# Performance work log

Measured on AMD Instinct MI355X. Metric: run time of the kernel, lower is better.

Reference implementation:

```python
import jax, jax.numpy as jnp
import numpy as np

N = 4096        # num_nodes == num_messages (required by the einsum contraction)
HID = 256       # hidden_dim
MD = 32         # message_dim (per-head dim)
H = 8           # num_heads


def setup_inputs() -> dict:
    key = jax.random.key(0)
    ks = jax.random.split(key, 12)
    s = 0.02
    return {
        "node_features": jax.random.normal(ks[0], (N, HID), dtype=jnp.float32),
        "messages": jax.random.normal(ks[1], (N, MD), dtype=jnp.float32),
        "adjacency": jax.random.randint(ks[2], (N, N), 0, 2, dtype=jnp.int32),
        "Wq": jax.random.normal(ks[3], (HID, H * MD), dtype=jnp.float32) * s,
        "bq": jnp.zeros((H * MD,), dtype=jnp.float32),
        "Wk": jax.random.normal(ks[4], (HID, H * MD), dtype=jnp.float32) * s,
        "bk": jnp.zeros((H * MD,), dtype=jnp.float32),
        "Wv": jax.random.normal(ks[5], (MD, H * MD), dtype=jnp.float32) * s,
        "bv": jnp.zeros((H * MD,), dtype=jnp.float32),
        "Wo": jax.random.normal(ks[6], (H * MD, MD), dtype=jnp.float32) * s,
        "bo": jnp.zeros((MD,), dtype=jnp.float32),
    }


def reference(node_features, messages, adjacency, Wq, bq, Wk, bk, Wv, bv, Wo, bo):
    n = node_features.shape[0]
    m = messages.shape[0]
    # projections; view(num, H, -1) splits the H*MD output as [H, MD]
    Q = (node_features @ Wq + bq).reshape(n, H, MD)   # [n, h, d]
    K = (node_features @ Wk + bk).reshape(n, H, MD)   # [m, h, d] (m == n)
    V = (messages @ Wv + bv).reshape(m, H, MD)        # [m, h, d]
    scale = 1.0 / np.sqrt(MD).astype(np.float32)
    scores = jnp.einsum('nhd,mhd->nmh', Q, K) * scale  # [n, m, h]
    # adjacency mask: masked_fill(mask == 0, -1e9)
    scores = jnp.where((adjacency == 0)[:, :, None], jnp.float32(-1e9), scores)
    attn = jax.nn.softmax(scores, axis=1)              # softmax over m
    routed = jnp.einsum('nmh,mhd->nhd', attn, V).reshape(n, H * MD)
    routed = routed @ Wo + bo                          # [n, MD]
    return routed, attn.mean(axis=-1)                  # ([n, MD], [n, m])
```

## Files before the change

### kernel.cpp

```cpp
#include <hip/hip_runtime.h>
#include <math.h>

#define NN 4096
#define HID 256
#define MD 32
#define NH 8
#define SCALE 0.17677669529663687f

typedef float f32x4 __attribute__((ext_vector_type(4)));
typedef short bf16x8 __attribute__((ext_vector_type(8)));
typedef _Float16 f16x4 __attribute__((ext_vector_type(4)));
typedef _Float16 f16x2 __attribute__((ext_vector_type(2)));

__device__ inline unsigned int bfr(float x) {
    unsigned int u = __float_as_uint(x);
    return (u + 0x7fffu + ((u >> 16) & 1u)) >> 16;
}
__device__ inline unsigned int pkbf(float a, float b) {
    return bfr(a) | (bfr(b) << 16);
}
__device__ inline unsigned int pkhf(float a, float b) {
    union { f16x2 h; unsigned int u; } z;
    z.h = (f16x2){(_Float16)a, (_Float16)b};
    return z.u;
}
__device__ inline unsigned int spread4(unsigned int x) {
    x = (x | (x << 12)) & 0x000F000Fu;
    x = (x | (x << 6))  & 0x03030303u;
    x = (x | (x << 3))  & 0x11111111u;
    return x;
}

__global__ __launch_bounds__(256) void prep_kernel(
    const float* __restrict__ nf, const float* __restrict__ Wq,
    const float* __restrict__ Wk, unsigned short* __restrict__ NFb,
    unsigned short* __restrict__ Wt)
{
    __shared__ __align__(16) float lds[64 * 65];
    const int b = blockIdx.x, t = threadIdx.x;
    if (b < 512) {
        const float* src = nf + (size_t)b * 2048 + t * 8;
        float4 a = ((const float4*)src)[0];
        float4 c = ((const float4*)src)[1];
        uint4 o;
        o.x = pkbf(a.x, a.y); o.y = pkbf(a.z, a.w);
        o.z = pkbf(c.x, c.y); o.w = pkbf(c.z, c.w);
        *(uint4*)(NFb + (size_t)b * 2048 + t * 8) = o;
        return;
    }
    const int b2 = b - 512;
    const int mat = b2 >> 4, tile = b2 & 15;
    const int k0 = (tile >> 2) * 64, c0 = (tile & 3) * 64;
    const float* W = mat ? Wk : Wq;
    #pragma unroll
    for (int i = 0; i < 16; ++i) {
        int idx = i * 256 + t;
        int row = idx >> 4, c4 = idx & 15;
        float4 v = *(const float4*)(W + (size_t)(k0 + row) * 256 + c0 + c4 * 4);
        lds[row * 65 + c4 * 4 + 0] = v.x;
        lds[row * 65 + c4 * 4 + 1] = v.y;
        lds[row * 65 + c4 * 4 + 2] = v.z;
        lds[row * 65 + c4 * 4 + 3] = v.w;
    }
    __syncthreads();
    #pragma unroll
    for (int i = 0; i < 2; ++i) {
        int j = i * 256 + t;
        int c_loc = j >> 3, kq = j & 7;
        uint4 o;
        o.x = pkbf(lds[(kq * 8 + 0) * 65 + c_loc], lds[(kq * 8 + 1) * 65 + c_loc]);
        o.y = pkbf(lds[(kq * 8 + 2) * 65 + c_loc], lds[(kq * 8 + 3) * 65 + c_loc]);
        o.z = pkbf(lds[(kq * 8 + 4) * 65 + c_loc], lds[(kq * 8 + 5) * 65 + c_loc]);
        o.w = pkbf(lds[(kq * 8 + 6) * 65 + c_loc], lds[(kq * 8 + 7) * 65 + c_loc]);
        *(uint4*)(Wt + (size_t)mat * 65536 + (size_t)(c0 + c_loc) * 256 + k0 + kq * 8) = o;
    }
}

__global__ __launch_bounds__(256, 4) void proj_mfma(
    const unsigned short* __restrict__ NFb, const unsigned short* __restrict__ Wt,
    const float* __restrict__ bq, const float* __restrict__ bk,
    unsigned short* __restrict__ Qb, unsigned short* __restrict__ Kb)
{
    const int b = blockIdx.x;
    const int isK = b >> 7, nb = b & 127;
    const unsigned short* Wm = Wt + (size_t)isK * 65536;
    const float* bias = isK ? bk : bq;
    unsigned short* outp = isK ? Kb : Qb;
    const int t = threadIdx.x, w = t >> 6, l = t & 63;
    const int g = l >> 4, q = l & 15;
    const int n0 = nb * 32 + (w & 1) * 16;
    const int chalf = w >> 1;

    f32x4 acc[8];
    #pragma unroll
    for (int ct = 0; ct < 8; ++ct) acc[ct] = (f32x4){0.f, 0.f, 0.f, 0.f};

    #pragma unroll
    for (int kc = 0; kc < 8; ++kc) {
        bf16x8 bfrag = *(const bf16x8*)(NFb + (size_t)(n0 + q) * 256 + kc * 32 + g * 8);
        #pragma unroll
        for (int ct = 0; ct < 8; ++ct) {
            int c = (chalf * 8 + ct) * 16 + q;
            bf16x8 afrag = *(const bf16x8*)(Wm + (size_t)c * 256 + kc * 32 + g * 8);
            acc[ct] = __builtin_amdgcn_mfma_f32_16x16x32_bf16(afrag, bfrag, acc[ct], 0, 0, 0);
        }
    }
    const float sc = isK ? 1.0f : SCALE;
    const int n = n0 + q;
    #pragma unroll
    for (int ct = 0; ct < 8; ++ct) {
        int c0 = (chalf * 8 + ct) * 16 + 4 * g;
        float4 bv = *(const float4*)(bias + c0);
        float v0 = (acc[ct][0] + bv.x) * sc;
        float v1 = (acc[ct][1] + bv.y) * sc;
        float v2 = (acc[ct][2] + bv.z) * sc;
        float v3 = (acc[ct][3] + bv.w) * sc;
        uint2 o;
        o.x = pkbf(v0, v1); o.y = pkbf(v2, v3);
        int h = c0 >> 5, d = c0 & 31;
        *(uint2*)(outp + ((size_t)h * NN + n) * 32 + d) = o;
    }
}

__global__ __launch_bounds__(256) void proj_v(
    const float* __restrict__ msg, const float* __restrict__ Wv,
    const float* __restrict__ bv, float* __restrict__ Vo)
{
    __shared__ __align__(16) float in_lds[32 * 32];
    const int nb = blockIdx.x;
    const int t = threadIdx.x;
    ((float4*)in_lds)[t] = ((const float4*)(msg + (size_t)nb * 1024))[t];
    __syncthreads();
    float acc[32];
    #pragma unroll
    for (int r = 0; r < 32; ++r) acc[r] = 0.f;
    #pragma unroll 8
    for (int k = 0; k < 32; ++k) {
        float w = Wv[k * 256 + t];
        #pragma unroll
        for (int r = 0; r < 32; ++r) acc[r] += in_lds[r * 32 + k] * w;
    }
    const float bb = bv[t];
    #pragma unroll
    for (int r = 0; r < 32; ++r)
        Vo[(size_t)(nb * 32 + r) * 256 + t] = acc[r] + bb;
}

__global__ __launch_bounds__(256) void abit_kernel(
    const int* __restrict__ adj, unsigned int* __restrict__ ab32)
{
    const int w = threadIdx.x >> 6, lane = threadIdx.x & 63;
    const int n = blockIdx.x * 4 + w;
    const int* base = adj + (size_t)n * NN;
    for (int it = 0; it < 16; ++it) {
        int4 v = *(const int4*)(base + it * 256 + lane * 4);
        unsigned long long b0 = __ballot(v.x != 0);
        unsigned long long b1 = __ballot(v.y != 0);
        unsigned long long b2 = __ballot(v.z != 0);
        unsigned long long b3 = __ballot(v.w != 0);
        if (lane < 8) {
            unsigned int sh = lane * 8;
            unsigned int B0 = (unsigned int)((b0 >> sh) & 0xffULL);
            unsigned int B1 = (unsigned int)((b1 >> sh) & 0xffULL);
            unsigned int B2 = (unsigned int)((b2 >> sh) & 0xffULL);
            unsigned int B3 = (unsigned int)((b3 >> sh) & 0xffULL);
            unsigned int wd = spread4(B0) | (spread4(B1) << 1)
                            | (spread4(B2) << 2) | (spread4(B3) << 3);
            ab32[(size_t)n * 128 + it * 8 + lane] = wd;
        }
    }
}

__global__ __launch_bounds__(256) void pack_vt(
    const float* __restrict__ Vf, unsigned short* __restrict__ Vt, int usef16)
{
    __shared__ __align__(16) float lds[128 * 33];
    const int h = blockIdx.x >> 5, mt = blockIdx.x & 31;
    const int t = threadIdx.x;
    for (int k = 0; k < 4; ++k) {
        int flat = k * 256 + t;
        int row = flat >> 3, c4 = flat & 7;
        float4 v = *(const float4*)(Vf + (size_t)(mt * 128 + row) * 256 + h * 32 + c4 * 4);
        lds[row * 33 + c4 * 4 + 0] = v.x;
        lds[row * 33 + c4 * 4 + 1] = v.y;
        lds[row * 33 + c4 * 4 + 2] = v.z;
        lds[row * 33 + c4 * 4 + 3] = v.w;
    }
    __syncthreads();
    const int d = t >> 3, mq = t & 7;
    #pragma unroll
    for (int k = 0; k < 2; ++k) {
        int m0 = mq * 16 + k * 8;
        uint4 o;
        if (usef16) {
            o.x = pkhf(lds[(m0 + 0) * 33 + d], lds[(m0 + 1) * 33 + d]);
            o.y = pkhf(lds[(m0 + 2) * 33 + d], lds[(m0 + 3) * 33 + d]);
            o.z = pkhf(lds[(m0 + 4) * 33 + d], lds[(m0 + 5) * 33 + d]);
            o.w = pkhf(lds[(m0 + 6) * 33 + d], lds[(m0 + 7) * 33 + d]);
        } else {
            o.x = pkbf(lds[(m0 + 0) * 33 + d], lds[(m0 + 1) * 33 + d]);
            o.y = pkbf(lds[(m0 + 2) * 33 + d], lds[(m0 + 3) * 33 + d]);
            o.z = pkbf(lds[(m0 + 4) * 33 + d], lds[(m0 + 5) * 33 + d]);
            o.w = pkbf(lds[(m0 + 6) * 33 + d], lds[(m0 + 7) * 33 + d]);
        }
        *(uint4*)(Vt + ((size_t)(h * 32 + d)) * NN + mt * 128 + m0) = o;
    }
}

__global__ __launch_bounds__(256, 4) void sweep1s_kernel(
    const unsigned short* __restrict__ Qb, const unsigned short* __restrict__ Kb,
    const unsigned int* __restrict__ abit, float* __restrict__ Lpart)
{
    __shared__ __align__(16) char smem[32768];
    const int nquad = blockIdx.x, msg = blockIdx.y;
    const int t = threadIdx.x;
    const int w = t >> 6, l = t & 63;
    const int g = l >> 4, q = l & 15;
    const int n0 = nquad * 64 + w * 16;
    const int m0 = msg * 512;
    const int fq = (q >> 1) & 3;

    const char* gsrc[4];
    #pragma unroll
    for (int i = 0; i < 4; ++i) {
        int s = i * 256 + t;
        int tile = s >> 7;
        int r = (s >> 2) & 31;
        int gr = (s & 3) ^ ((r >> 1) & 3);
        gsrc[i] = (const char*)Kb + (((size_t)tile * NN + m0 + r) * 64 + gr * 16);
    }
    const unsigned int* abrow = abit + (size_t)(n0 + q) * 128 + msg * 16;

    bf16x8 qf[8];
    #pragma unroll
    for (int h = 0; h < 8; ++h)
        qf[h] = *(const bf16x8*)(Qb + (((size_t)h * NN + n0 + q) << 5) + g * 8);
    float lacc[8];
    #pragma unroll
    for (int h = 0; h < 8; ++h) lacc[h] = 0.f;

    #pragma unroll
    for (int i = 0; i < 4; ++i)
        __builtin_amdgcn_global_load_lds((const unsigned int*)gsrc[i],
            (unsigned int*)(smem + i * 4096 + w * 1024), 16, 0, 0);
    unsigned int wb = abrow[0];
    unsigned int wbn = 0;
    __syncthreads();

    for (int c = 0; c < 16; ++c) {
        const char* cur = smem + (c & 1) * 16384;
        if (c < 15) {
            wbn = abrow[c + 1];
            char* nxt = smem + ((c & 1) ^ 1) * 16384;
            #pragma unroll
            for (int i = 0; i < 4; ++i)
                __builtin_amdgcn_global_load_lds(
                    (const unsigned int*)(gsrc[i] + (size_t)(c + 1) * 2048),
                    (unsigned int*)(nxt + i * 4096 + w * 1024), 16, 0, 0);
        }
        #pragma unroll
        for (int h = 0; h < 8; ++h) {
            const int ko = h * 2048 + q * 64 + ((g ^ fq) << 4);
            bf16x8 ka0 = *(const bf16x8*)(cur + ko);
            bf16x8 ka1 = *(const bf16x8*)(cur + ko + 1024);
            f32x4 z = {0.f, 0.f, 0.f, 0.f};
            f32x4 s0 = __builtin_amdgcn_mfma_f32_16x16x32_bf16(ka0, qf[h], z, 0, 0, 0);
            f32x4 s1 = __builtin_amdgcn_mfma_f32_16x16x32_bf16(ka1, qf[h], z, 0, 0, 0);
            #pragma unroll
            for (int r = 0; r < 4; ++r) {
                float e0 = __expf(s0[r]);
                float e1 = __expf(s1[r]);
                lacc[h] += ((wb >> (4 * g + r)) & 1u) ? e0 : 0.f;
                lacc[h] += ((wb >> (16 + 4 * g + r)) & 1u) ? e1 : 0.f;
            }
        }
        __syncthreads();
        wb = wbn;
    }
    #pragma unroll
    for (int h = 0; h < 8; ++h) {
        float v = lacc[h];
        v += __shfl_xor(v, 16);
        v += __shfl_xor(v, 32);
        if (g == 0) Lpart[(size_t)msg * 32768 + h * NN + n0 + q] = v;
    }
}

__global__ __launch_bounds__(256, 2) void sweep2s_kernel(
    const unsigned short* __restrict__ Qb, const unsigned short* __restrict__ Kb,
    const unsigned short* __restrict__ Vt, const unsigned int* __restrict__ abit,
    const float* __restrict__ Linv, float* __restrict__ Opart,
    float* __restrict__ amean)
{
    __shared__ __align__(16) char smem[65536];
    const int nquad = blockIdx.x, msg = blockIdx.y;
    const int t = threadIdx.x;
    const int w = t >> 6, l = t & 63;
    const int g = l >> 4, q = l & 15;
    const int n0 = nquad * 64 + w * 16;
    const int m0 = msg * 512;
    const int fq = (q >> 1) & 3;

    const char* gsrc[8];
    unsigned int gstep[8];
    #pragma unroll
    for (int i = 0; i < 8; ++i) {
        int s = i * 256 + t;
        int tile = s >> 7;
        int r = (s >> 2) & 31;
        int gr = (s & 3) ^ ((r >> 1) & 3);
        if (tile < 8) {
            gsrc[i] = (const char*)Kb + (((size_t)tile * NN + m0 + r) * 64 + gr * 16);
            gstep[i] = 2048;
        } else {
            gsrc[i] = (const char*)Vt + ((((size_t)(tile - 8) * 32 + r) * NN + m0) * 2 + gr * 16);
            gstep[i] = 64;
        }
    }
    const unsigned int* abrow = abit + (size_t)(n0 + q) * 128 + msg * 16;

    bf16x8 qf[8];
    float rL[8];
    #pragma unroll
    for (int h = 0; h < 8; ++h) {
        qf[h] = *(const bf16x8*)(Qb + (((size_t)h * NN + n0 + q) << 5) + g * 8);
        rL[h] = Linv[h * NN + n0 + q];
    }
    f32x4 o[8][2];
    #pragma unroll
    for (int h = 0; h < 8; ++h) {
        o[h][0] = (f32x4){0.f, 0.f, 0.f, 0.f};
        o[h][1] = (f32x4){0.f, 0.f, 0.f, 0.f};
    }

    #pragma unroll
    for (int i = 0; i < 8; ++i)
        __builtin_amdgcn_global_load_lds((const unsigned int*)gsrc[i],
            (unsigned int*)(smem + i * 4096 + w * 1024), 16, 0, 0);
    unsigned int wb = abrow[0];
    unsigned int wbn = 0;
    __syncthreads();

    for (int c = 0; c < 16; ++c) {
        const char* cur = smem + (c & 1) * 32768;
        if (c < 15) {
            wbn = abrow[c + 1];
            char* nxt = smem + ((c & 1) ^ 1) * 32768;
            #pragma unroll
            for (int i = 0; i < 8; ++i)
                __builtin_amdgcn_global_load_lds(
                    (const unsigned int*)(gsrc[i] + (size_t)(c + 1) * gstep[i]),
                    (unsigned int*)(nxt + i * 4096 + w * 1024), 16, 0, 0);
        }
        const int mb = m0 + c * 32;
        float am[8];
        #pragma unroll
        for (int r = 0; r < 8; ++r) am[r] = 0.f;

        #pragma unroll
        for (int h = 0; h < 8; ++h) {
            const int ko = h * 2048 + q * 64 + ((g ^ fq) << 4);
            bf16x8 ka0 = *(const bf16x8*)(cur + ko);
            bf16x8 ka1 = *(const bf16x8*)(cur + ko + 1024);
            const int vbase = (8 + h) * 2048 + q * 64 + (g & 1) * 8;
            const int vo0 = vbase + (((g >> 1) ^ fq) << 4);
            const int vo1 = vbase + (((2 + (g >> 1)) ^ fq) << 4);
            f16x4 va00 = *(const f16x4*)(cur + vo0);
            f16x4 va01 = *(const f16x4*)(cur + vo0 + 1024);
            f16x4 va10 = *(const f16x4*)(cur + vo1);
            f16x4 va11 = *(const f16x4*)(cur + vo1 + 1024);
            f32x4 z = {0.f, 0.f, 0.f, 0.f};
            f32x4 s0 = __builtin_amdgcn_mfma_f32_16x16x32_bf16(ka0, qf[h], z, 0, 0, 0);
            f32x4 s1 = __builtin_amdgcn_mfma_f32_16x16x32_bf16(ka1, qf[h], z, 0, 0, 0);
            float pn[8];
            #pragma unroll
            for (int r = 0; r < 4; ++r) {
                float e0 = __expf(s0[r]) * rL[h];
                float e1 = __expf(s1[r]) * rL[h];
                pn[r]     = ((wb >> (4 * g + r)) & 1u) ? e0 : 0.f;
                pn[4 + r] = ((wb >> (16 + 4 * g + r)) & 1u) ? e1 : 0.f;
                am[r] += pn[r];
                am[4 + r] += pn[4 + r];
            }
            union { unsigned int u[2]; f16x4 v; } pA, pB;
            pA.u[0] = pkhf(pn[0], pn[1]); pA.u[1] = pkhf(pn[2], pn[3]);
            pB.u[0] = pkhf(pn[4], pn[5]); pB.u[1] = pkhf(pn[6], pn[7]);
            o[h][0] = __builtin_amdgcn_mfma_f32_16x16x16f16(va00, pA.v, o[h][0], 0, 0, 0);
            o[h][1] = __builtin_amdgcn_mfma_f32_16x16x16f16(va01, pA.v, o[h][1], 0, 0, 0);
            o[h][0] = __builtin_amdgcn_mfma_f32_16x16x16f16(va10, pB.v, o[h][0], 0, 0, 0);
            o[h][1] = __builtin_amdgcn_mfma_f32_16x16x16f16(va11, pB.v, o[h][1], 0, 0, 0);
        }
        float4 a0, a1;
        a0.x = am[0] * 0.125f; a0.y = am[1] * 0.125f;
        a0.z = am[2] * 0.125f; a0.w = am[3] * 0.125f;
        a1.x = am[4] * 0.125f; a1.y = am[5] * 0.125f;
        a1.z = am[6] * 0.125f; a1.w = am[7] * 0.125f;
        *(float4*)(amean + (size_t)(n0 + q) * NN + mb + 4 * g) = a0;
        *(float4*)(amean + (size_t)(n0 + q) * NN + mb + 16 + 4 * g) = a1;
        __syncthreads();
        wb = wbn;
    }

    float* op = Opart + ((size_t)msg * NN + n0 + q) * 256;
    #pragma unroll
    for (int h = 0; h < 8; ++h) {
        *(f32x4*)(op + h * 32 + 4 * g) = o[h][0];
        *(f32x4*)(op + h * 32 + 16 + 4 * g) = o[h][1];
    }
}

__global__ __launch_bounds__(256, 4) void sweep1_old(
    const unsigned short* __restrict__ Qb, const unsigned short* __restrict__ Kb,
    const unsigned int* __restrict__ abit, float* __restrict__ Lpart)
{
    const int ntile = blockIdx.x, msg = blockIdx.y;
    const int t = threadIdx.x;
    const int w = t >> 6, l = t & 63;
    const int g = l >> 4, q = l & 15;
    const int ms = msg * 4 + w;
    const int n0 = ntile * 16;
    const int mbase = ms * 256;
    bf16x8 qf[8];
    #pragma unroll
    for (int h = 0; h < 8; ++h)
        qf[h] = *(const bf16x8*)(Qb + (((size_t)h * NN + n0 + q) << 5) + g * 8);
    float lacc[8];
    #pragma unroll
    for (int h = 0; h < 8; ++h) lacc[h] = 0.f;
    for (int ch = 0; ch < 8; ++ch) {
        const int mb = mbase + ch * 32;
        const unsigned int wbits = abit[(size_t)(n0 + q) * 128 + (mb >> 5)];
        #pragma unroll
        for (int h = 0; h < 8; ++h) {
            bf16x8 ka0 = *(const bf16x8*)(Kb + (((size_t)h * NN + mb + q) << 5) + g * 8);
            bf16x8 ka1 = *(const bf16x8*)(Kb + (((size_t)h * NN + mb + 16 + q) << 5) + g * 8);
            f32x4 z = {0.f, 0.f, 0.f, 0.f};
            f32x4 s0 = __builtin_amdgcn_mfma_f32_16x16x32_bf16(ka0, qf[h], z, 0, 0, 0);
            f32x4 s1 = __builtin_amdgcn_mfma_f32_16x16x32_bf16(ka1, qf[h], z, 0, 0, 0);
            #pragma unroll
            for (int r = 0; r < 4; ++r) {
                float e0 = __expf(s0[r]);
                float e1 = __expf(s1[r]);
                lacc[h] += ((wbits >> (4 * g + r)) & 1u) ? e0 : 0.f;
                lacc[h] += ((wbits >> (16 + 4 * g + r)) & 1u) ? e1 : 0.f;
            }
        }
    }
    #pragma unroll
    for (int h = 0; h < 8; ++h) {
        float v = lacc[h];
        v += __shfl_xor(v, 16);
        v += __shfl_xor(v, 32);
        if (g == 0) Lpart[(size_t)ms * 32768 + h * NN + n0 + q] = v;
    }
}

__global__ __launch_bounds__(256, 2) void sweep2_old(
    const unsigned short* __restrict__ Qb, const unsigned short* __restrict__ Kb,
    const unsigned short* __restrict__ Vt, const unsigned int* __restrict__ abit,
    const float* __restrict__ Linv, float* __restrict__ Opart,
    float* __restrict__ amean)
{
    __shared__ __align__(16) float Ow[2 * 16 * 260];
    const int ntile = blockIdx.x, msg = blockIdx.y;
    const int t = threadIdx.x;
    const int w = t >> 6, l = t & 63;
    const int g = l >> 4, q = l & 15;
    const int ms = msg * 4 + w;
    const int n0 = ntile * 16;
    const int mbase = ms * 256;
    const int baddr = (q + (g & 1) * 32) << 2;
    const bool hi = (g >= 2);
    bf16x8 qf[8];
    float rL[8];
    #pragma unroll
    for (int h = 0; h < 8; ++h) {
        qf[h] = *(const bf16x8*)(Qb + (((size_t)h * NN + n0 + q) << 5) + g * 8);
        rL[h] = Linv[h * NN + n0 + q];
    }
    f32x4 o[8][2];
    #pragma unroll
    for (int h = 0; h < 8; ++h) {
        o[h][0] = (f32x4){0.f, 0.f, 0.f, 0.f};
        o[h][1] = (f32x4){0.f, 0.f, 0.f, 0.f};
    }
    for (int ch = 0; ch < 8; ++ch) {
        const int mb = mbase + ch * 32;
        const unsigned int wbits = abit[(size_t)(n0 + q) * 128 + (mb >> 5)];
        float am[8];
        #pragma unroll
        for (int r = 0; r < 8; ++r) am[r] = 0.f;
        #pragma unroll
        for (int h = 0; h < 8; ++h) {
            bf16x8 ka0 = *(const bf16x8*)(Kb + (((size_t)h * NN + mb + q) << 5) + g * 8);
            bf16x8 ka1 = *(const bf16x8*)(Kb + (((size_t)h * NN + mb + 16 + q) << 5) + g * 8);
            f32x4 z = {0.f, 0.f, 0.f, 0.f};
            f32x4 s0 = __builtin_amdgcn_mfma_f32_16x16x32_bf16(ka0, qf[h], z, 0, 0, 0);
            f32x4 s1 = __builtin_amdgcn_mfma_f32_16x16x32_bf16(ka1, qf[h], z, 0, 0, 0);
            float pn[8];
            #pragma unroll
            for (int r = 0; r < 4; ++r) {
                float e0 = __expf(s0[r]) * rL[h];
                float e1 = __expf(s1[r]) * rL[h];
                pn[r]     = ((wbits >> (4 * g + r)) & 1u) ? e0 : 0.f;
                pn[4 + r] = ((wbits >> (16 + 4 * g + r)) & 1u) ? e1 : 0.f;
                am[r] += pn[r];
                am[4 + r] += pn[4 + r];
            }
            unsigned int pk0 = pkbf(pn[0], pn[1]);
            unsigned int pk1 = pkbf(pn[2], pn[3]);
            unsigned int pk2 = pkbf(pn[4], pn[5]);
            unsigned int pk3 = pkbf(pn[6], pn[7]);
            int r0lo = __builtin_amdgcn_ds_bpermute(baddr,      (int)pk0);
            int r0hi = __builtin_amdgcn_ds_bpermute(baddr,      (int)pk2);
            int r1lo = __builtin_amdgcn_ds_bpermute(baddr,      (int)pk1);
            int r1hi = __builtin_amdgcn_ds_bpermute(baddr,      (int)pk3);
            int r2lo = __builtin_amdgcn_ds_bpermute(baddr + 64, (int)pk0);
            int r2hi = __builtin_amdgcn_ds_bpermute(baddr + 64, (int)pk2);
            int r3lo = __builtin_amdgcn_ds_bpermute(baddr + 64, (int)pk1);
            int r3hi = __builtin_amdgcn_ds_bpermute(baddr + 64, (int)pk3);
            union { unsigned int u[4]; bf16x8 v; } pu;
            pu.u[0] = (unsigned int)(hi ? r0hi : r0lo);
            pu.u[1] = (unsigned int)(hi ? r1hi : r1lo);
            pu.u[2] = (unsigned int)(hi ? r2hi : r2lo);
            pu.u[3] = (unsigned int)(hi ? r3hi : r3lo);
            bf16x8 va0 = *(const bf16x8*)(Vt + ((size_t)(h * 32 + q)) * NN + mb + g * 8);
            bf16x8 va1 = *(const bf16x8*)(Vt + ((size_t)(h * 32 + 16 + q)) * NN + mb + g * 8);
            o[h][0] = __builtin_amdgcn_mfma_f32_16x16x32_bf16(va0, pu.v, o[h][0], 0, 0, 0);
            o[h][1] = __builtin_amdgcn_mfma_f32_16x16x32_bf16(va1, pu.v, o[h][1], 0, 0, 0);
        }
        float4 a0, a1;
        a0.x = am[0] * 0.125f; a0.y = am[1] * 0.125f;
        a0.z = am[2] * 0.125f; a0.w = am[3] * 0.125f;
        a1.x = am[4] * 0.125f; a1.y = am[5] * 0.125f;
        a1.z = am[6] * 0.125f; a1.w = am[7] * 0.125f;
        *(float4*)(amean + (size_t)(n0 + q) * NN + mb + 4 * g) = a0;
        *(float4*)(amean + (size_t)(n0 + q) * NN + mb + 16 + 4 * g) = a1;
    }
    if (w < 2) {
        #pragma unroll
        for (int h = 0; h < 8; ++h)
            #pragma unroll
            for (int dt = 0; dt < 2; ++dt)
                *(f32x4*)&Ow[w * 4160 + q * 260 + h * 32 + dt * 16 + 4 * g] = o[h][dt];
    }
    __syncthreads();
    if (w >= 2) {
        #pragma unroll
        for (int h = 0; h < 8; ++h)
            #pragma unroll
            for (int dt = 0; dt < 2; ++dt) {
                f32x4* p = (f32x4*)&Ow[(w - 2) * 4160 + q * 260 + h * 32 + dt * 16 + 4 * g];
                *p = *p + o[h][dt];
            }
    }
    __syncthreads();
    for (int i = t; i < 4096; i += 256) {
        int n = i >> 8, c2 = i & 255;
        float v = Ow[n * 260 + c2] + Ow[4160 + n * 260 + c2];
        Opart[((size_t)msg * NN + n0 + n) * 256 + c2] = v;
    }
}

__global__ __launch_bounds__(256) void linv_kernel(
    const float* __restrict__ Lpart, float* __restrict__ Linv, int nms)
{
    int i = blockIdx.x * 256 + threadIdx.x;
    float s = 0.f;
    for (int ms = 0; ms < nms; ++ms) s += Lpart[(size_t)ms * 32768 + i];
    Linv[i] = 1.0f / s;
}

__global__ __launch_bounds__(256) void final_kernel(
    const float* __restrict__ Opart, const float* __restrict__ Wo,
    const float* __restrict__ bo, float* __restrict__ routed, int nms)
{
    __shared__ __align__(16) float Osum[16 * 260];
    __shared__ __align__(16) float WoT[32 * 260];
    const int nb = blockIdx.x, t = threadIdx.x;
    for (int i4 = t; i4 < 2048; i4 += 256) {
        int k = i4 >> 3, j4b = i4 & 7;
        float4 v = *(const float4*)(Wo + k * 32 + j4b * 4);
        WoT[(j4b * 4 + 0) * 260 + k] = v.x;
        WoT[(j4b * 4 + 1) * 260 + k] = v.y;
        WoT[(j4b * 4 + 2) * 260 + k] = v.z;
        WoT[(j4b * 4 + 3) * 260 + k] = v.w;
    }
    for (int i = t; i < 4096; i += 256) {
        int r = i >> 8, c = i & 255;
        const float* ap = Opart + ((size_t)(nb * 16 + r)) * 256 + c;
        float s = 0.f;
        for (int ms = 0; ms < nms; ++ms) s += ap[(size_t)ms * 1048576];
        Osum[r * 260 + c] = s;
    }
    __syncthreads();
    const int rh = t >> 5, j = t & 31;
    const float bj = bo[j];
    #pragma unroll
    for (int rr = 0; rr < 2; ++rr) {
        int r = rh * 2 + rr;
        float a0 = 0.f, a1 = 0.f;
        #pragma unroll
        for (int i4 = 0; i4 < 64; i4 += 2) {
            float4 ov = *(const float4*)&Osum[r * 260 + i4 * 4];
            float4 wv = *(const float4*)&WoT[j * 260 + i4 * 4];
            a0 += ov.x * wv.x + ov.y * wv.y + ov.z * wv.z + ov.w * wv.w;
            float4 ov2 = *(const float4*)&Osum[r * 260 + i4 * 4 + 4];
            float4 wv2 = *(const float4*)&WoT[j * 260 + i4 * 4 + 4];
            a1 += ov2.x * wv2.x + ov2.y * wv2.y + ov2.z * wv2.z + ov2.w * wv2.w;
        }
        routed[(size_t)(nb * 16 + r) * 32 + j] = a0 + a1 + bj;
    }
}

extern "C" void kernel_launch(void* const* d_in, const int* in_sizes, int n_in,
                              void* d_out, int out_size, void* d_ws, size_t ws_size,
                              hipStream_t stream) {
    const float* nf  = (const float*)d_in[0];
    const float* msg = (const float*)d_in[1];
    const int*   adj = (const int*)d_in[2];
    const float* Wq  = (const float*)d_in[3];
    const float* bq  = (const float*)d_in[4];
    const float* Wk  = (const float*)d_in[5];
    const float* bk  = (const float*)d_in[6];
    const float* Wv  = (const float*)d_in[7];
    const float* bv  = (const float*)d_in[8];
    const float* Wo  = (const float*)d_in[9];
    const float* bo  = (const float*)d_in[10];

    float* routed = (float*)d_out;
    float* amean  = (float*)d_out + (size_t)NN * MD;
    float* ws = (float*)d_ws;

    const bool bigws = (ws_size >= 43122688ull);

    if (bigws) {
        float* Vf = ws;
        unsigned short* NFb = (unsigned short*)(ws + 2097152);
        unsigned short* Wt  = (unsigned short*)(ws + 2621440);
        float* Opart = ws;
        unsigned short* Qb = (unsigned short*)(ws + 8388608);
        unsigned short* Kb = (unsigned short*)(ws + 8912896);
        unsigned short* Vt = (unsigned short*)(ws + 9437184);
        unsigned int*   ab32 = (unsigned int*)(ws + 9961472);
        float* Lpart = ws + 10485760;
        float* Linv  = ws + 10747904;

        prep_kernel<<<544, 256, 0, stream>>>(nf, Wq, Wk, NFb, Wt);
        proj_mfma<<<256, 256, 0, stream>>>(NFb, Wt, bq, bk, Qb, Kb);
        proj_v<<<128, 256, 0, stream>>>(msg, Wv, bv, Vf);
        abit_kernel<<<1024, 256, 0, stream>>>(adj, ab32);
        pack_vt<<<256, 256, 0, stream>>>(Vf, Vt, 1);
        sweep1s_kernel<<<dim3(64, 8), 256, 0, stream>>>(Qb, Kb, ab32, Lpart);
        linv_kernel<<<128, 256, 0, stream>>>(Lpart, Linv, 8);
        sweep2s_kernel<<<dim3(64, 8), 256, 0, stream>>>(Qb, Kb, Vt, ab32, Linv, Opart, amean);
        final_kernel<<<256, 256, 0, stream>>>(Opart, Wo, bo, routed, 8);
    } else {
        float* Vf = ws;
        unsigned short* NFb = (unsigned short*)(ws + 2097152);
        unsigned short* Wt  = (unsigned short*)(ws + 2621440);
        float* Opart = ws;
        unsigned short* Qb = (unsigned short*)(ws + 4194304);
        unsigned short* Kb = (unsigned short*)(ws + 4718592);
        unsigned short* Vt = (unsigned short*)(ws + 5242880);
        unsigned int*   ab32 = (unsigned int*)(ws + 5767168);
        float* Lpart = ws + 6291456;
        float* Linv  = ws + 6815744;

        prep_kernel<<<544, 256, 0, stream>>>(nf, Wq, Wk, NFb, Wt);
        proj_mfma<<<256, 256, 0, stream>>>(NFb, Wt, bq, bk, Qb, Kb);
        proj_v<<<128, 256, 0, stream>>>(msg, Wv, bv, Vf);
        abit_kernel<<<1024, 256, 0, stream>>>(adj, ab32);
        pack_vt<<<256, 256, 0, stream>>>(Vf, Vt, 0);
        sweep1_old<<<dim3(256, 4), 256, 0, stream>>>(Qb, Kb, ab32, Lpart);
        linv_kernel<<<128, 256, 0, stream>>>(Lpart, Linv, 16);
        sweep2_old<<<dim3(256, 4), 256, 0, stream>>>(Qb, Kb, Vt, ab32, Linv, Opart, amean);
        final_kernel<<<256, 256, 0, stream>>>(Opart, Wo, bo, routed, 4);
    }
}
```

Before: 175.1 us.

## Fold log2e into Q scale and split sweep2 m-tiles across 512-thread blocks

Q projection is scaled by log2(e)/sqrt(d) so softmax exponentials can use exp2f instead of __expf, removing a multiply per score. The second sweep kernel now launches 512 threads where pairs of waves split the 32-message chunk in half, each doing one score MFMA and two PV MFMAs per head. The two partial outputs are reduced through shared memory before the store. This is meant to raise wave-level parallelism and lower per-wave register pressure, at the cost of an extra LDS reduction, an extra barrier and a larger shared buffer.

```diff
diff --git a/kernel.cpp b/kernel.cpp
--- a/kernel.cpp
+++ b/kernel.cpp
@@ -6,6 +6,7 @@
 #define MD 32
 #define NH 8
 #define SCALE 0.17677669529663687f
+#define QSCALE 0.25503164588f
 
 typedef float f32x4 __attribute__((ext_vector_type(4)));
 typedef short bf16x8 __attribute__((ext_vector_type(8)));
@@ -105,7 +106,7 @@
             acc[ct] = __builtin_amdgcn_mfma_f32_16x16x32_bf16(afrag, bfrag, acc[ct], 0, 0, 0);
         }
     }
-    const float sc = isK ? 1.0f : SCALE;
+    const float sc = isK ? 1.0f : QSCALE;
     const int n = n0 + q;
     #pragma unroll
     for (int ct = 0; ct < 8; ++ct) {
@@ -268,8 +269,8 @@
             f32x4 s1 = __builtin_amdgcn_mfma_f32_16x16x32_bf16(ka1, qf[h], z, 0, 0, 0);
             #pragma unroll
             for (int r = 0; r < 4; ++r) {
-                float e0 = __expf(s0[r]);
-                float e1 = __expf(s1[r]);
+                float e0 = exp2f(s0[r]);
+                float e1 = exp2f(s1[r]);
                 lacc[h] += ((wb >> (4 * g + r)) & 1u) ? e0 : 0.f;
                 lacc[h] += ((wb >> (16 + 4 * g + r)) & 1u) ? e1 : 0.f;
             }
@@ -286,26 +287,27 @@
     }
 }
 
-__global__ __launch_bounds__(256, 2) void sweep2s_kernel(
+__global__ __launch_bounds__(512, 4) void sweep2s_kernel(
     const unsigned short* __restrict__ Qb, const unsigned short* __restrict__ Kb,
     const unsigned short* __restrict__ Vt, const unsigned int* __restrict__ abit,
     const float* __restrict__ Linv, float* __restrict__ Opart,
     float* __restrict__ amean)
 {
-    __shared__ __align__(16) char smem[65536];
+    __shared__ __align__(16) char smem[69632];
     const int nquad = blockIdx.x, msg = blockIdx.y;
     const int t = threadIdx.x;
     const int w = t >> 6, l = t & 63;
     const int g = l >> 4, q = l & 15;
-    const int n0 = nquad * 64 + w * 16;
+    const int nt = w >> 1, msub = w & 1;
+    const int n0 = nquad * 64 + nt * 16;
     const int m0 = msg * 512;
     const int fq = (q >> 1) & 3;
 
-    const char* gsrc[8];
-    unsigned int gstep[8];
-    #pragma unroll
-    for (int i = 0; i < 8; ++i) {
-        int s = i * 256 + t;
+    const char* gsrc[4];
+    unsigned int gstep[4];
+    #pragma unroll
+    for (int i = 0; i < 4; ++i) {
+        int s = i * 512 + t;
         int tile = s >> 7;
         int r = (s >> 2) & 31;
         int gr = (s & 3) ^ ((r >> 1) & 3);
@@ -334,12 +336,16 @@
     }
 
     #pragma unroll
-    for (int i = 0; i < 8; ++i)
+    for (int i = 0; i < 4; ++i)
         __builtin_amdgcn_global_load_lds((const unsigned int*)gsrc[i],
-            (unsigned int*)(smem + i * 4096 + w * 1024), 16, 0, 0);
+            (unsigned int*)(smem + i * 8192 + w * 1024), 16, 0, 0);
     unsigned int wb = abrow[0];
     unsigned int wbn = 0;
     __syncthreads();
+
+    const int kbase = q * 64 + ((g ^ fq) << 4) + msub * 1024;
+    const int vbase = q * 64 + (g & 1) * 8 + (((msub * 2 + (g >> 1)) ^ fq) << 4);
+    const int shift = msub * 16 + 4 * g;
 
     for (int c = 0; c < 16; ++c) {
         const char* cur = smem + (c & 1) * 32768;
@@ -347,65 +353,62 @@
             wbn = abrow[c + 1];
             char* nxt = smem + ((c & 1) ^ 1) * 32768;
             #pragma unroll
-            for (int i = 0; i < 8; ++i)
+            for (int i = 0; i < 4; ++i)
                 __builtin_amdgcn_global_load_lds(
                     (const unsigned int*)(gsrc[i] + (size_t)(c + 1) * gstep[i]),
-                    (unsigned int*)(nxt + i * 4096 + w * 1024), 16, 0, 0);
+                    (unsigned int*)(nxt + i * 8192 + w * 1024), 16, 0, 0);
         }
         const int mb = m0 + c * 32;
-        float am[8];
-        #pragma unroll
-        for (int r = 0; r < 8; ++r) am[r] = 0.f;
+        float am[4];
+        #pragma unroll
+        for (int r = 0; r < 4; ++r) am[r] = 0.f;
 
         #pragma unroll
         for (int h = 0; h < 8; ++h) {
-            const int ko = h * 2048 + q * 64 + ((g ^ fq) << 4);
-            bf16x8 ka0 = *(const bf16x8*)(cur + ko);
-            bf16x8 ka1 = *(const bf16x8*)(cur + ko + 1024);
-            const int vbase = (8 + h) * 2048 + q * 64 + (g & 1) * 8;
-            const int vo0 = vbase + (((g >> 1) ^ fq) << 4);
-            const int vo1 = vbase + (((2 + (g >> 1)) ^ fq) << 4);
-            f16x4 va00 = *(const f16x4*)(cur + vo0);
-            f16x4 va01 = *(const f16x4*)(cur + vo0 + 1024);
-            f16x4 va10 = *(const f16x4*)(cur + vo1);
-            f16x4 va11 = *(const f16x4*)(cur + vo1 + 1024);
+            bf16x8 ka = *(const bf16x8*)(cur + h * 2048 + kbase);
+            const char* vrow = cur + (8 + h) * 2048 + vbase;
+            f16x4 va0 = *(const f16x4*)(vrow);
+            f16x4 va1 = *(const f16x4*)(vrow + 1024);
             f32x4 z = {0.f, 0.f, 0.f, 0.f};
-            f32x4 s0 = __builtin_amdgcn_mfma_f32_16x16x32_bf16(ka0, qf[h], z, 0, 0, 0);
-            f32x4 s1 = __builtin_amdgcn_mfma_f32_16x16x32_bf16(ka1, qf[h], z, 0, 0, 0);
-            float pn[8];
+            f32x4 s0 = __builtin_amdgcn_mfma_f32_16x16x32_bf16(ka, qf[h], z, 0, 0, 0);
+            float pn[4];
             #pragma unroll
             for (int r = 0; r < 4; ++r) {
-                float e0 = __expf(s0[r]) * rL[h];
-                float e1 = __expf(s1[r]) * rL[h];
-                pn[r]     = ((wb >> (4 * g + r)) & 1u) ? e0 : 0.f;
-                pn[4 + r] = ((wb >> (16 + 4 * g + r)) & 1u) ? e1 : 0.f;
+                float e0 = exp2f(s0[r]) * rL[h];
+                pn[r] = ((wb >> (shift + r)) & 1u) ? e0 : 0.f;
                 am[r] += pn[r];
-                am[4 + r] += pn[4 + r];
             }
-            union { unsigned int u[2]; f16x4 v; } pA, pB;
+            union { unsigned int u[2]; f16x4 v; } pA;
             pA.u[0] = pkhf(pn[0], pn[1]); pA.u[1] = pkhf(pn[2], pn[3]);
-            pB.u[0] = pkhf(pn[4], pn[5]); pB.u[1] = pkhf(pn[6], pn[7]);
-            o[h][0] = __builtin_amdgcn_mfma_f32_16x16x16f16(va00, pA.v, o[h][0], 0, 0, 0);
-            o[h][1] = __builtin_amdgcn_mfma_f32_16x16x16f16(va01, pA.v, o[h][1], 0, 0, 0);
-            o[h][0] = __builtin_amdgcn_mfma_f32_16x16x16f16(va10, pB.v, o[h][0], 0, 0, 0);
-            o[h][1] = __builtin_amdgcn_mfma_f32_16x16x16f16(va11, pB.v, o[h][1], 0, 0, 0);
-        }
-        float4 a0, a1;
+            o[h][0] = __builtin_amdgcn_mfma_f32_16x16x16f16(va0, pA.v, o[h][0], 0, 0, 0);
+            o[h][1] = __builtin_amdgcn_mfma_f32_16x16x16f16(va1, pA.v, o[h][1], 0, 0, 0);
+        }
+        float4 a0;
         a0.x = am[0] * 0.125f; a0.y = am[1] * 0.125f;
         a0.z = am[2] * 0.125f; a0.w = am[3] * 0.125f;
-        a1.x = am[4] * 0.125f; a1.y = am[5] * 0.125f;
-        a1.z = am[6] * 0.125f; a1.w = am[7] * 0.125f;
-        *(float4*)(amean + (size_t)(n0 + q) * NN + mb + 4 * g) = a0;
-        *(float4*)(amean + (size_t)(n0 + q) * NN + mb + 16 + 4 * g) = a1;
+        *(float4*)(amean + (size_t)(n0 + q) * NN + mb + msub * 16 + 4 * g) = a0;
         __syncthreads();
         wb = wbn;
     }
 
-    float* op = Opart + ((size_t)msg * NN + n0 + q) * 256;
-    #pragma unroll
-    for (int h = 0; h < 8; ++h) {
-        *(f32x4*)(op + h * 32 + 4 * g) = o[h][0];
-        *(f32x4*)(op + h * 32 + 16 + 4 * g) = o[h][1];
+    float* red = (float*)smem + nt * 4352;
+    if (msub == 0) {
+        #pragma unroll
+        for (int h = 0; h < 8; ++h) {
+            *(f32x4*)(red + q * 260 + h * 32 + 4 * g) = o[h][0];
+            *(f32x4*)(red + q * 260 + h * 32 + 16 + 4 * g) = o[h][1];
+        }
+    }
+    __syncthreads();
+    if (msub == 1) {
+        float* op = Opart + ((size_t)msg * NN + n0 + q) * 256;
+        #pragma unroll
+        for (int h = 0; h < 8; ++h) {
+            f32x4 v0 = *(f32x4*)(red + q * 260 + h * 32 + 4 * g) + o[h][0];
+            f32x4 v1 = *(f32x4*)(red + q * 260 + h * 32 + 16 + 4 * g) + o[h][1];
+            *(f32x4*)(op + h * 32 + 4 * g) = v0;
+            *(f32x4*)(op + h * 32 + 16 + 4 * g) = v1;
+        }
     }
 }
 
@@ -439,8 +442,8 @@
             f32x4 s1 = __builtin_amdgcn_mfma_f32_16x16x32_bf16(ka1, qf[h], z, 0, 0, 0);
             #pragma unroll
             for (int r = 0; r < 4; ++r) {
-                float e0 = __expf(s0[r]);
-                float e1 = __expf(s1[r]);
+                float e0 = exp2f(s0[r]);
+                float e1 = exp2f(s1[r]);
                 lacc[h] += ((wbits >> (4 * g + r)) & 1u) ? e0 : 0.f;
                 lacc[h] += ((wbits >> (16 + 4 * g + r)) & 1u) ? e1 : 0.f;
             }
@@ -500,8 +503,8 @@
             float pn[8];
             #pragma unroll
             for (int r = 0; r < 4; ++r) {
-                float e0 = __expf(s0[r]) * rL[h];
-                float e1 = __expf(s1[r]) * rL[h];
+                float e0 = exp2f(s0[r]) * rL[h];
+                float e1 = exp2f(s1[r]) * rL[h];
                 pn[r]     = ((wbits >> (4 * g + r)) & 1u) ? e0 : 0.f;
                 pn[4 + r] = ((wbits >> (16 + 4 * g + r)) & 1u) ? e1 : 0.f;
                 am[r] += pn[r];
@@ -653,7 +656,7 @@
         pack_vt<<<256, 256, 0, stream>>>(Vf, Vt, 1);
         sweep1s_kernel<<<dim3(64, 8), 256, 0, stream>>>(Qb, Kb, ab32, Lpart);
         linv_kernel<<<128, 256, 0, stream>>>(Lpart, Linv, 8);
-        sweep2s_kernel<<<dim3(64, 8), 256, 0, stream>>>(Qb, Kb, Vt, ab32, Linv, Opart, amean);
+        sweep2s_kernel<<<dim3(64, 8), 512, 0, stream>>>(Qb, Kb, Vt, ab32, Linv, Opart, amean);
         final_kernel<<<256, 256, 0, stream>>>(Opart, Wo, bo, routed, 8);
     } else {
         float* Vf = ws;
```

Measured after the change: 342.2 us. 95.5% more time.
